# Performance work log

Hardware: AMD Instinct MI355X
Metric: run time of the kernel (lower is better)

Reference implementation:

```python
import jax, jax.numpy as jnp
import numpy as np

B, E, S, D = 32, 64, 50, 300   # batch, sentences/essay, words/sentence, word dim
F = 100                        # conv filters (cnn_lstm_convunits_size)
H = 100                        # lstm units (cnn_lstm_att_pool_size)
W_WIN = 5                      # word window length


def setup_inputs() -> dict:
    key = jax.random.key(0)
    ks = jax.random.split(key, 12)
    n = lambda k, shape: (jax.random.normal(k, shape, jnp.float32) * 0.05)
    return {
        "essays": jax.random.normal(ks[0], (B, E, S, D), jnp.float32),
        "conv_k": n(ks[1], (1, W_WIN, D, F)),      # HWIO
        "conv_b": jnp.zeros((F,), jnp.float32),
        "att1_mat": n(ks[2], (F, F)),
        "att1_bias": n(ks[3], (F,)),
        "att1_vec": n(ks[4], (F, 1)),
        "lstm_W": n(ks[5], (F + H, 4 * H)),        # TF BasicLSTMCell kernel, gate order i,j,f,o
        "lstm_b": jnp.zeros((4 * H,), jnp.float32),
        "att2_mat": n(ks[6], (H, H)),
        "att2_bias": n(ks[7], (H,)),
        "att2_vec": n(ks[8], (H, 1)),
        "dense_w": n(ks[9], (H, 1)),
        "dense_b": jnp.zeros((1,), jnp.float32),
    }


def reference(essays, conv_k, conv_b, att1_mat, att1_bias, att1_vec,
              lstm_W, lstm_b, att2_mat, att2_bias, att2_vec,
              dense_w, dense_b):
    # conv2d, kernel [1, w_window_len], SAME padding, relu  -> [B,E,S,F]
    conv1 = jax.lax.conv_general_dilated(
        essays, conv_k, window_strides=(1, 1), padding="SAME",
        dimension_numbers=("NHWC", "HWIO", "NHWC"))
    conv1 = jax.nn.relu(conv1 + conv_b)

    # attention pooling over words (axis=2)
    a1 = jnp.tanh(jnp.einsum("besf,fg->besg", conv1, att1_mat) + att1_bias)
    a1 = jnp.einsum("besg,go->beso", a1, att1_vec)          # [B,E,S,1]
    a1 = jax.nn.softmax(a1, axis=2)
    sent = jnp.sum(a1 * conv1, axis=2)                       # [B,E,F]

    # BasicLSTMCell (forget_bias=1.0, gate order i,j,f,o) over sentence axis
    hdim = lstm_b.shape[0] // 4
    bsz = essays.shape[0]

    def step(carry, xt):
        c, h = carry
        z = jnp.concatenate([xt, h], axis=1) @ lstm_W + lstm_b
        i, j, f, o = jnp.split(z, 4, axis=1)
        c = c * jax.nn.sigmoid(f + 1.0) + jax.nn.sigmoid(i) * jnp.tanh(j)
        h = jax.nn.sigmoid(o) * jnp.tanh(c)
        return (c, h), h

    init = (jnp.zeros((bsz, hdim), sent.dtype), jnp.zeros((bsz, hdim), sent.dtype))
    xs = jnp.swapaxes(sent, 0, 1)                            # [E,B,F]
    _, hs = jax.lax.scan(step, init, xs)
    lstm = jnp.swapaxes(hs, 0, 1)                            # [B,E,H]

    # attention pooling over sentences (axis=1)
    a2 = jnp.tanh(jnp.einsum("beh,hg->beg", lstm, att2_mat) + att2_bias)
    a2 = jnp.einsum("beg,go->beo", a2, att2_vec)             # [B,E,1]
    a2 = jax.nn.softmax(a2, axis=1)
    essay_repr = jnp.sum(a2 * lstm, axis=1)                  # [B,H]

    preds = jax.nn.sigmoid(essay_repr @ dense_w + dense_b).reshape(-1)  # [B]
    return preds
```

## Files before the change

### kernel.cpp

```cpp
#include <hip/hip_runtime.h>
#include <hip/hip_bf16.h>
#include <stdint.h>

#define Bsz 32
#define Esz 64
#define Ssz 50
#define Dsz 300
#define Fsz 100
#define Hsz 100
#define WWIN 5

#define PX   328
#define PC   136
#define KT_CONV 50
#define NTILES  7
#define NGRP 2214

typedef __attribute__((ext_vector_type(8))) short bf16x8;
typedef __attribute__((ext_vector_type(8))) unsigned short u16x8;
typedef __attribute__((ext_vector_type(4))) float f32x4;
typedef _Float16 half2_t __attribute__((ext_vector_type(2)));

union UH32 { unsigned int u; half2_t v; };
union UH16 { _Float16 h; unsigned short u; };

__device__ __forceinline__ float sigmoid_fast(float x) {
    return 1.0f / (1.0f + __expf(-x));
}
__device__ __forceinline__ float tanhf_fast(float x) {
    const float ax = fabsf(x);
    const float e = __expf(2.0f * ax);
    const float t = 1.0f - 2.0f / (e + 1.0f);
    return copysignf(t, x);
}

__device__ __forceinline__ unsigned short f2bf(float x) {
    union { __hip_bfloat16 h; unsigned short u; } cv;
    cv.h = __float2bfloat16(x);
    return cv.u;
}
__device__ __forceinline__ unsigned int f2bf2(float lo, float hi) {
    union { __hip_bfloat162 h2; unsigned int u; } cv;
    cv.h2 = __float22bfloat162_rn(make_float2(lo, hi));
    return cv.u;
}
__device__ __forceinline__ float bf2f(unsigned short b) {
    union { uint32_t u; float f; } v; v.u = ((uint32_t)b) << 16;
    return v.f;
}
__device__ __forceinline__ float dpp_bcast(float z, const int sel) {
    int r;
    switch (sel) {
        case 0: r = __builtin_amdgcn_mov_dpp(__builtin_bit_cast(int, z), 0x00, 0xf, 0xf, false); break;
        case 1: r = __builtin_amdgcn_mov_dpp(__builtin_bit_cast(int, z), 0x55, 0xf, 0xf, false); break;
        case 2: r = __builtin_amdgcn_mov_dpp(__builtin_bit_cast(int, z), 0xaa, 0xf, 0xf, false); break;
        default: r = __builtin_amdgcn_mov_dpp(__builtin_bit_cast(int, z), 0xff, 0xf, 0xf, false); break;
    }
    return __builtin_bit_cast(float, r);
}

#define N_BTGC (KT_CONV * 112 * 32)
#define N_BTGA (4 * 112 * 32)
#define N_BTGW (4 * 400 * 32)
#define N_BTGP (52 * 400)

__global__ __launch_bounds__(256) void prep_kernel(
    const float* __restrict__ conv_k, const float* __restrict__ att1_mat,
    const float* __restrict__ lstm_W,
    unsigned short* __restrict__ BtgC, unsigned short* __restrict__ BtgA,
    unsigned short* __restrict__ BtgW, unsigned int* __restrict__ BtgP)
{
    const int total = N_BTGC + N_BTGA + N_BTGW + N_BTGP;
    for (int i = blockIdx.x * 256 + threadIdx.x; i < total; i += gridDim.x * 256) {
        if (i < N_BTGC) {
            const int kt = i / (112 * 32);
            const int r  = i % (112 * 32);
            const int n  = r / 32;
            const int kk = r % 32;
            const int w  = kt / 10;
            const int d  = (kt % 10) * 32 + kk;
            float val = (d < Dsz && n < Fsz) ? conv_k[((size_t)w * Dsz + d) * Fsz + n] : 0.f;
            BtgC[i] = f2bf(val);
        } else if (i < N_BTGC + N_BTGA) {
            const int j  = i - N_BTGC;
            const int kt = j / (112 * 32);
            const int r  = j % (112 * 32);
            const int n  = r / 32;
            const int kk = r % 32;
            const int k  = kt * 32 + kk;
            float val = (k < Fsz && n < Fsz) ? att1_mat[(size_t)k * Fsz + n] : 0.f;
            BtgA[j] = f2bf(val);
        } else if (i < N_BTGC + N_BTGA + N_BTGW) {
            const int j  = i - N_BTGC - N_BTGA;
            const int kt = j / (400 * 32);
            const int r  = j % (400 * 32);
            const int n  = r / 32;
            const int kk = r % 32;
            const int k  = kt * 32 + kk;
            float val = (k < Fsz) ? lstm_W[(size_t)k * 400 + n] : 0.f;
            BtgW[j] = f2bf(val);
        } else {
            const int j   = i - N_BTGC - N_BTGA - N_BTGW;
            const int k2  = j / 400;
            const int col = j - k2 * 400;
            const int gate = col & 3;
            const int cell = col >> 2;
            const int src  = gate * 100 + cell;
            const int k0 = 2 * k2, k1 = 2 * k2 + 1;
            const float v0 = (k0 < Hsz) ? lstm_W[(size_t)(Fsz + k0) * 400 + src] : 0.f;
            const float v1 = (k1 < Hsz) ? lstm_W[(size_t)(Fsz + k1) * 400 + src] : 0.f;
            union { _Float16 h[2]; unsigned int u; } cv;
            cv.h[0] = (_Float16)v0;
            cv.h[1] = (_Float16)v1;
            BtgP[j] = cv.u;
        }
    }
}

template<int KT>
__device__ __forceinline__ void cv_loadB(
    const unsigned short* __restrict__ BtgC, const int (&boffs)[7], bf16x8 (&b)[7])
{
#pragma unroll
    for (int nt = 0; nt < 7; ++nt)
        b[nt] = *reinterpret_cast<const bf16x8*>(BtgC + KT * 3584 + boffs[nt]);
}

template<int KT>
__device__ __forceinline__ void cv_loadA(
    const unsigned short* b0p, const unsigned short* b1p, int abase, bf16x8 (&a)[2])
{
    constexpr int off = (KT / 10) * PX + (KT % 10) * 32;
    a[0] = *reinterpret_cast<const bf16x8*>(&b0p[abase + off]);
    a[1] = *reinterpret_cast<const bf16x8*>(&b1p[abase + off]);
}

__device__ __forceinline__ void cv_mfma(
    const bf16x8 (&a)[2], const bf16x8 (&b)[7], f32x4 (&acc)[2][7])
{
    __builtin_amdgcn_s_setprio(1);
#pragma unroll
    for (int nt = 0; nt < 7; ++nt) {
        acc[0][nt] = __builtin_amdgcn_mfma_f32_16x16x32_bf16(a[0], b[nt], acc[0][nt], 0, 0, 0);
        acc[1][nt] = __builtin_amdgcn_mfma_f32_16x16x32_bf16(a[1], b[nt], acc[1][nt], 0, 0, 0);
    }
    __builtin_amdgcn_s_setprio(0);
}

template<int KT>
struct CvLoop {
    static __device__ __forceinline__ void run(
        const unsigned short* __restrict__ BtgC, const int (&boffs)[7],
        const unsigned short* b0p, const unsigned short* b1p, int abase,
        bf16x8 (&B0)[7], bf16x8 (&B1)[7], bf16x8 (&B2)[7],
        bf16x8 (&aX)[2], bf16x8 (&aY)[2], f32x4 (&acc)[2][7])
    {
        if constexpr (KT + 1 < KT_CONV) {
            if constexpr ((KT & 1) == 0) cv_loadA<KT + 1>(b0p, b1p, abase, aY);
            else                         cv_loadA<KT + 1>(b0p, b1p, abase, aX);
        }
        if constexpr (KT + 2 < KT_CONV) {
            if constexpr ((KT + 2) % 3 == 0)      cv_loadB<KT + 2>(BtgC, boffs, B0);
            else if constexpr ((KT + 2) % 3 == 1) cv_loadB<KT + 2>(BtgC, boffs, B1);
            else                                  cv_loadB<KT + 2>(BtgC, boffs, B2);
        }
        if constexpr ((KT & 1) == 0) {
            if constexpr (KT % 3 == 0)      cv_mfma(aX, B0, acc);
            else if constexpr (KT % 3 == 1) cv_mfma(aX, B1, acc);
            else                            cv_mfma(aX, B2, acc);
        } else {
            if constexpr (KT % 3 == 0)      cv_mfma(aY, B0, acc);
            else if constexpr (KT % 3 == 1) cv_mfma(aY, B1, acc);
            else                            cv_mfma(aY, B2, acc);
        }
        CvLoop<KT + 1>::run(BtgC, boffs, b0p, b1p, abase, B0, B1, B2, aX, aY, acc);
    }
};
template<>
struct CvLoop<KT_CONV> {
    static __device__ __forceinline__ void run(
        const unsigned short* __restrict__, const int (&)[7],
        const unsigned short*, const unsigned short*, int,
        bf16x8 (&)[7], bf16x8 (&)[7], bf16x8 (&)[7],
        bf16x8 (&)[2], bf16x8 (&)[2], f32x4 (&)[2][7]) {}
};

__global__ __launch_bounds__(256, 2) void conv_att1_kernel(
    const float* __restrict__ essays,
    const unsigned short* __restrict__ BtgC,
    const unsigned short* __restrict__ BtgA,
    const float* __restrict__ conv_b,
    const float* __restrict__ att1_bias,
    const float* __restrict__ att1_vec,
    unsigned short* __restrict__ sent_bf)
{
    __shared__ __align__(16) unsigned short buf[2][54 * PX];
    __shared__ float u_s[2][64];
    __shared__ float alpha_s[2][64];

    const int be0 = blockIdx.x * 2;
    const int tid = threadIdx.x;
    const int lane = tid & 63;
    const int wid  = tid >> 6;
    const int ln   = lane & 15;
    const int qd   = lane >> 4;

    if (tid < 128) u_s[tid >> 6][tid & 63] = 0.f;

    const int m = wid * 16 + ln;
    const int abase = (m < Ssz ? m : Ssz - 1) * PX + 8 * qd;

    int boffs[7];
#pragma unroll
    for (int nt = 0; nt < 7; ++nt) boffs[nt] = (nt * 16 + ln) * 32 + 8 * qd;

    bf16x8 B0[7], B1[7], B2[7];
    cv_loadB<0>(BtgC, boffs, B0);
    cv_loadB<1>(BtgC, boffs, B1);

#pragma unroll
    for (int es = 0; es < 2; ++es) {
        const float* in_g = essays + (size_t)(be0 + es) * (Ssz * Dsz);
        float4 va[9], vb[9];
        int rr[9], cc[9];
        bool hv[9], fv[9], gv[9];
#pragma unroll
        for (int it = 0; it < 9; ++it) {
            const int g  = tid + it * 256;
            const int r  = g / 41;
            const int c8 = (g - r * 41) * 8;
            const int s  = r - 2;
            gv[it] = (g < NGRP);
            hv[it] = gv[it] && (s >= 0) && (s < Ssz) && (c8 < Dsz);
            fv[it] = hv[it] && (c8 + 8 <= Dsz);
            const float* base = in_g + (hv[it] ? (s * Dsz + c8) : 0);
            va[it] = *reinterpret_cast<const float4*>(base);
            vb[it] = *reinterpret_cast<const float4*>(fv[it] ? base + 4 : base);
            rr[it] = r; cc[it] = c8;
        }
#pragma unroll
        for (int it = 0; it < 9; ++it) {
            if (!gv[it]) continue;
            const float e0 = hv[it] ? va[it].x : 0.f;
            const float e1 = hv[it] ? va[it].y : 0.f;
            const float e2 = hv[it] ? va[it].z : 0.f;
            const float e3 = hv[it] ? va[it].w : 0.f;
            const float e4 = fv[it] ? vb[it].x : 0.f;
            const float e5 = fv[it] ? vb[it].y : 0.f;
            const float e6 = fv[it] ? vb[it].z : 0.f;
            const float e7 = fv[it] ? vb[it].w : 0.f;
            uint4 o;
            o.x = f2bf2(e0, e1);
            o.y = f2bf2(e2, e3);
            o.z = f2bf2(e4, e5);
            o.w = f2bf2(e6, e7);
            *reinterpret_cast<uint4*>(&buf[es][rr[it] * PX + cc[it]]) = o;
        }
    }
    __syncthreads();

    const unsigned short* b0p = buf[0];
    const unsigned short* b1p = buf[1];

    f32x4 acc[2][7];
#pragma unroll
    for (int es = 0; es < 2; ++es)
#pragma unroll
        for (int nt = 0; nt < 7; ++nt) acc[es][nt] = (f32x4)0.f;

    {
        bf16x8 aX[2], aY[2];
        cv_loadA<0>(b0p, b1p, abase, aX);
        CvLoop<0>::run(BtgC, boffs, b0p, b1p, abase, B0, B1, B2, aX, aY, acc);
    }
    __syncthreads();

#pragma unroll
    for (int nt = 0; nt < 7; ++nt) {
        const int n_g = nt * 16 + ln;
        const float bias = (n_g < Fsz) ? conv_b[n_g] : 0.f;
#pragma unroll
        for (int es = 0; es < 2; ++es) {
#pragma unroll
            for (int j = 0; j < 4; ++j) {
                const int m_row = wid * 16 + qd * 4 + j;
                buf[es][m_row * PC + n_g] = f2bf(fmaxf(acc[es][nt][j] + bias, 0.f));
            }
        }
    }
    for (int idx = tid; idx < 2 * 64 * 2; idx += 256) {
        const int es = idx >> 7;
        const int r2 = idx & 127;
        const int row = r2 >> 1;
        const int c = 112 + (r2 & 1) * 8;
        *reinterpret_cast<u16x8*>(&buf[es][row * PC + c]) = (u16x8)0;
    }
    __syncthreads();

    f32x4 acc2[2][7];
#pragma unroll
    for (int es = 0; es < 2; ++es)
#pragma unroll
        for (int nt = 0; nt < 7; ++nt) acc2[es][nt] = (f32x4)0.f;

    const int abase2 = (wid * 16 + ln) * PC + 8 * qd;
#pragma unroll
    for (int kt = 0; kt < 4; ++kt) {
        bf16x8 a[2];
        a[0] = *reinterpret_cast<const bf16x8*>(&b0p[abase2 + kt * 32]);
        a[1] = *reinterpret_cast<const bf16x8*>(&b1p[abase2 + kt * 32]);
        bf16x8 bb[7];
#pragma unroll
        for (int nt = 0; nt < 7; ++nt)
            bb[nt] = *reinterpret_cast<const bf16x8*>(BtgA + kt * 3584 + boffs[nt]);
        __builtin_amdgcn_s_setprio(1);
#pragma unroll
        for (int nt = 0; nt < 7; ++nt) {
            acc2[0][nt] = __builtin_amdgcn_mfma_f32_16x16x32_bf16(a[0], bb[nt], acc2[0][nt], 0, 0, 0);
            acc2[1][nt] = __builtin_amdgcn_mfma_f32_16x16x32_bf16(a[1], bb[nt], acc2[1][nt], 0, 0, 0);
        }
        __builtin_amdgcn_s_setprio(0);
    }

    {
        float bias_v[7], vec_v[7];
#pragma unroll
        for (int nt = 0; nt < 7; ++nt) {
            const int g = nt * 16 + ln;
            const bool ok = (g < Fsz);
            bias_v[nt] = ok ? att1_bias[g] : 0.f;
            vec_v[nt]  = ok ? att1_vec[g]  : 0.f;
        }
#pragma unroll
        for (int es = 0; es < 2; ++es) {
#pragma unroll
            for (int j = 0; j < 4; ++j) {
                const int m_row = wid * 16 + qd * 4 + j;
                float val = 0.f;
                if (m_row < Ssz) {
#pragma unroll
                    for (int nt = 0; nt < 7; ++nt) {
                        const int g = nt * 16 + ln;
                        if (g < Fsz)
                            val += tanhf_fast(acc2[es][nt][j] + bias_v[nt]) * vec_v[nt];
                    }
                }
                val += __shfl_xor(val, 1);
                val += __shfl_xor(val, 2);
                val += __shfl_xor(val, 4);
                val += __shfl_xor(val, 8);
                if (ln == 0 && m_row < Ssz) atomicAdd(&u_s[es][m_row], val);
            }
        }
    }
    __syncthreads();

    if (wid < 2) {
        const float uv = (lane < Ssz) ? u_s[wid][lane] : -1e30f;
        float m2 = uv;
#pragma unroll
        for (int off = 32; off > 0; off >>= 1) m2 = fmaxf(m2, __shfl_xor(m2, off));
        float e = (lane < Ssz) ? __expf(uv - m2) : 0.f;
        float sum = e;
#pragma unroll
        for (int off = 32; off > 0; off >>= 1) sum += __shfl_xor(sum, off);
        alpha_s[wid][lane] = e / sum;
    }
    __syncthreads();

    {
        const int es = tid >> 7;
        const int f  = tid & 127;
        unsigned short v = 0;
        if (f < Fsz) {
            float a = 0.f;
            for (int s = 0; s < Ssz; ++s) a += alpha_s[es][s] * bf2f(buf[es][s * PC + f]);
            v = f2bf(a);
        }
        sent_bf[(size_t)(be0 + es) * 128 + f] = v;
    }
}

__global__ __launch_bounds__(256) void xpart_kernel(
    const unsigned short* __restrict__ sent_bf,
    const unsigned short* __restrict__ BtgW,
    const float* __restrict__ lstm_b,
    float* __restrict__ xpartB)
{
    const int wid  = threadIdx.x >> 6;
    const int mt   = blockIdx.x * 4 + wid;
    const int lane = threadIdx.x & 63;
    const int ln   = lane & 15;
    const int qd   = lane >> 4;
    const int m0   = mt * 16;

    f32x4 acc[25];
#pragma unroll
    for (int nt = 0; nt < 25; ++nt) acc[nt] = (f32x4)0.f;

#pragma unroll
    for (int kt = 0; kt < 4; ++kt) {
        const bf16x8 a = *reinterpret_cast<const bf16x8*>(
            sent_bf + (size_t)(m0 + ln) * 128 + kt * 32 + 8 * qd);
#pragma unroll
        for (int nt = 0; nt < 25; ++nt) {
            const bf16x8 b = *reinterpret_cast<const bf16x8*>(
                BtgW + ((size_t)kt * 400 + nt * 16 + ln) * 32 + 8 * qd);
            acc[nt] = __builtin_amdgcn_mfma_f32_16x16x32_bf16(a, b, acc[nt], 0, 0, 0);
        }
    }

#pragma unroll
    for (int nt = 0; nt < 25; ++nt) {
        const int col = nt * 16 + ln;
        const int gate = col / 100;
        const int cell = col - gate * 100;
        const float bias = lstm_b[col];
        const int gi = cell * 4 + gate;
#pragma unroll
        for (int j = 0; j < 4; ++j) {
            const int row = m0 + qd * 4 + j;
            xpartB[(size_t)row * 400 + gi] = acc[nt][j] + bias;
        }
    }
}

__global__ __launch_bounds__(448) void lstm_att2_kernel(
    const float* __restrict__ xpartB,
    const unsigned int* __restrict__ BtgP,
    const float* __restrict__ att2_mat,
    const float* __restrict__ att2_bias,
    const float* __restrict__ att2_vec,
    const float* __restrict__ dense_w,
    const float* __restrict__ dense_b,
    float* __restrict__ out)
{
    __shared__ __align__(16) float xp_lds[Esz * 400];
    __shared__ __align__(16) float hist[Esz * Hsz];
    __shared__ __align__(16) unsigned short h16[2][104];
    __shared__ float u2_s[Esz];
    __shared__ float alpha2_s[Esz];
    __shared__ float repr_s[Hsz];

    const int b   = blockIdx.x;
    const int tid = threadIdx.x;
    const bool actv = tid < 400;
    const int cell = tid >> 2;
    const int g    = tid & 3;

    {
        const float4* src = reinterpret_cast<const float4*>(xpartB + (size_t)b * Esz * 400);
        float4* dst = reinterpret_cast<float4*>(xp_lds);
        for (int i = tid; i < Esz * 100; i += 448) dst[i] = src[i];
    }

    unsigned int wp[52];
    if (actv) {
#pragma unroll
        for (int q = 0; q < 52; ++q) wp[q] = BtgP[q * 400 + tid];
    }
    if (tid < 104) { h16[0][tid] = 0; h16[1][tid] = 0; }
    float c = 0.f;
    __syncthreads();

    for (int t = 0; t < Esz; ++t) {
        float z = 0.f;
        if (actv) {
            const uint4* hq = reinterpret_cast<const uint4*>(h16[t & 1]);
            float za = xp_lds[t * 400 + tid], zb = 0.f, zc = 0.f, zd = 0.f;
#pragma unroll
            for (int q = 0; q < 13; ++q) {
                const uint4 hv = hq[q];
                UH32 h0, h1, h2, h3, w0, w1, w2, w3;
                h0.u = hv.x; h1.u = hv.y; h2.u = hv.z; h3.u = hv.w;
                w0.u = wp[4 * q + 0]; w1.u = wp[4 * q + 1];
                w2.u = wp[4 * q + 2]; w3.u = wp[4 * q + 3];
                za = __builtin_amdgcn_fdot2(w0.v, h0.v, za, false);
                zb = __builtin_amdgcn_fdot2(w1.v, h1.v, zb, false);
                zc = __builtin_amdgcn_fdot2(w2.v, h2.v, zc, false);
                zd = __builtin_amdgcn_fdot2(w3.v, h3.v, zd, false);
            }
            z = (za + zb) + (zc + zd);

            const float zi = dpp_bcast(z, 0);
            const float zj = dpp_bcast(z, 1);
            const float zf = dpp_bcast(z, 2);
            const float zo = dpp_bcast(z, 3);

            c = c * sigmoid_fast(zf + 1.0f) + sigmoid_fast(zi) * tanhf_fast(zj);
            const float h = sigmoid_fast(zo) * tanhf_fast(c);
            if (g == 0) {
                UH16 cv; cv.h = (_Float16)h;
                h16[(t + 1) & 1][cell] = cv.u;
                hist[t * Hsz + cell] = h;
            }
        }
        __syncthreads();
    }

    float* w2_s = xp_lds;
    for (int idx = tid; idx < Esz * Hsz; idx += 448) {
        const int e = idx / Hsz;
        const int gg = idx - e * Hsz;
        const float* lp = hist + e * Hsz;
        float a0 = 0.f, a1 = 0.f, a2 = 0.f, a3 = 0.f;
        for (int k = 0; k < Hsz; k += 4) {
            a0 += lp[k + 0] * att2_mat[(k + 0) * Hsz + gg];
            a1 += lp[k + 1] * att2_mat[(k + 1) * Hsz + gg];
            a2 += lp[k + 2] * att2_mat[(k + 2) * Hsz + gg];
            a3 += lp[k + 3] * att2_mat[(k + 3) * Hsz + gg];
        }
        w2_s[idx] = tanhf_fast(att2_bias[gg] + ((a0 + a1) + (a2 + a3))) * att2_vec[gg];
    }
    __syncthreads();

    if (tid < Esz) {
        float acc = 0.f;
        const float* wpp = w2_s + tid * Hsz;
        for (int gg = 0; gg < Hsz; ++gg) acc += wpp[gg];
        u2_s[tid] = acc;
    }
    __syncthreads();

    if (tid < 64) {
        const float uv = u2_s[tid];
        float m = uv;
#pragma unroll
        for (int off = 32; off > 0; off >>= 1) m = fmaxf(m, __shfl_xor(m, off));
        float e = __expf(uv - m);
        float sum = e;
#pragma unroll
        for (int off = 32; off > 0; off >>= 1) sum += __shfl_xor(sum, off);
        alpha2_s[tid] = e / sum;
    }
    __syncthreads();

    if (tid < Hsz) {
        float acc = 0.f;
        for (int e = 0; e < Esz; ++e) acc += alpha2_s[e] * hist[e * Hsz + tid];
        repr_s[tid] = acc;
    }
    __syncthreads();

    if (tid == 0) {
        float acc = dense_b[0];
        for (int hh = 0; hh < Hsz; ++hh) acc += repr_s[hh] * dense_w[hh];
        out[b] = sigmoid_fast(acc);
    }
}

extern "C" void kernel_launch(void* const* d_in, const int* in_sizes, int n_in,
                              void* d_out, int out_size, void* d_ws, size_t ws_size,
                              hipStream_t stream) {
    const float* essays    = (const float*)d_in[0];
    const float* conv_k    = (const float*)d_in[1];
    const float* conv_b    = (const float*)d_in[2];
    const float* att1_mat  = (const float*)d_in[3];
    const float* att1_bias = (const float*)d_in[4];
    const float* att1_vec  = (const float*)d_in[5];
    const float* lstm_W    = (const float*)d_in[6];
    const float* lstm_b    = (const float*)d_in[7];
    const float* att2_mat  = (const float*)d_in[8];
    const float* att2_bias = (const float*)d_in[9];
    const float* att2_vec  = (const float*)d_in[10];
    const float* dense_w   = (const float*)d_in[11];
    const float* dense_b   = (const float*)d_in[12];

    float* out = (float*)d_out;

    char* ws = (char*)d_ws;
    unsigned short* sent_bf = (unsigned short*)ws;
    float* xpartB = (float*)(ws + 524288);
    unsigned short* BtgC = (unsigned short*)(ws + 3801088);
    unsigned short* BtgA = (unsigned short*)(ws + 4159488);
    unsigned short* BtgW = (unsigned short*)(ws + 4188160);
    unsigned int*   BtgP = (unsigned int*)(ws + 4290560);

    prep_kernel<<<512, 256, 0, stream>>>(conv_k, att1_mat, lstm_W, BtgC, BtgA, BtgW, BtgP);
    conv_att1_kernel<<<Bsz * Esz / 2, 256, 0, stream>>>(
        essays, BtgC, BtgA, conv_b, att1_bias, att1_vec, sent_bf);
    xpart_kernel<<<32, 256, 0, stream>>>(sent_bf, BtgW, lstm_b, xpartB);
    lstm_att2_kernel<<<Bsz, 448, 0, stream>>>(
        xpartB, BtgP, att2_mat, att2_bias, att2_vec, dense_w, dense_b, out);
}
```

Before: 223.9 us.

## Retile conv MFMA to 2x2 wave grid and halve LSTM threads per cell

The conv and att1 GEMMs move from each wave owning a 16-row M strip across 7 N tiles to a 2x2 wave grid. Each wave now owns 32 rows by 64 columns, with N padded to 128. This cuts redundant B-fragment loads per wave and raises A reuse, but adds padded columns and more accumulator registers. Separately, the LSTM recurrence kernel uses 2 threads per cell, each computing two gates, instead of 4. Gates are exchanged with a single DPP pair swap, and the block shrinks from 448 to 256 threads, which lowers the cost of the per-step barrier but doubles the dot-product work per thread.

```diff
diff --git a/kernel.cpp b/kernel.cpp
--- a/kernel.cpp
+++ b/kernel.cpp
@@ -13,7 +13,6 @@
 #define PX   328
 #define PC   136
 #define KT_CONV 50
-#define NTILES  7
 #define NGRP 2214
 
 typedef __attribute__((ext_vector_type(8))) short bf16x8;
@@ -48,19 +47,13 @@
     union { uint32_t u; float f; } v; v.u = ((uint32_t)b) << 16;
     return v.f;
 }
-__device__ __forceinline__ float dpp_bcast(float z, const int sel) {
-    int r;
-    switch (sel) {
-        case 0: r = __builtin_amdgcn_mov_dpp(__builtin_bit_cast(int, z), 0x00, 0xf, 0xf, false); break;
-        case 1: r = __builtin_amdgcn_mov_dpp(__builtin_bit_cast(int, z), 0x55, 0xf, 0xf, false); break;
-        case 2: r = __builtin_amdgcn_mov_dpp(__builtin_bit_cast(int, z), 0xaa, 0xf, 0xf, false); break;
-        default: r = __builtin_amdgcn_mov_dpp(__builtin_bit_cast(int, z), 0xff, 0xf, 0xf, false); break;
-    }
+__device__ __forceinline__ float dpp_swap_pair(float z) {
+    int r = __builtin_amdgcn_mov_dpp(__builtin_bit_cast(int, z), 0xB1, 0xf, 0xf, false);
     return __builtin_bit_cast(float, r);
 }
 
-#define N_BTGC (KT_CONV * 112 * 32)
-#define N_BTGA (4 * 112 * 32)
+#define N_BTGC (KT_CONV * 128 * 32)
+#define N_BTGA (4 * 128 * 32)
 #define N_BTGW (4 * 400 * 32)
 #define N_BTGP (52 * 400)
 
@@ -73,8 +66,8 @@
     const int total = N_BTGC + N_BTGA + N_BTGW + N_BTGP;
     for (int i = blockIdx.x * 256 + threadIdx.x; i < total; i += gridDim.x * 256) {
         if (i < N_BTGC) {
-            const int kt = i / (112 * 32);
-            const int r  = i % (112 * 32);
+            const int kt = i / (128 * 32);
+            const int r  = i % (128 * 32);
             const int n  = r / 32;
             const int kk = r % 32;
             const int w  = kt / 10;
@@ -83,8 +76,8 @@
             BtgC[i] = f2bf(val);
         } else if (i < N_BTGC + N_BTGA) {
             const int j  = i - N_BTGC;
-            const int kt = j / (112 * 32);
-            const int r  = j % (112 * 32);
+            const int kt = j / (128 * 32);
+            const int r  = j % (128 * 32);
             const int n  = r / 32;
             const int kk = r % 32;
             const int k  = kt * 32 + kk;
@@ -119,41 +112,48 @@
 
 template<int KT>
 __device__ __forceinline__ void cv_loadB(
-    const unsigned short* __restrict__ BtgC, const int (&boffs)[7], bf16x8 (&b)[7])
+    const unsigned short* __restrict__ BtgC, const int (&boffs)[4], bf16x8 (&b)[4])
 {
 #pragma unroll
-    for (int nt = 0; nt < 7; ++nt)
-        b[nt] = *reinterpret_cast<const bf16x8*>(BtgC + KT * 3584 + boffs[nt]);
+    for (int i = 0; i < 4; ++i)
+        b[i] = *reinterpret_cast<const bf16x8*>(BtgC + KT * 4096 + boffs[i]);
 }
 
 template<int KT>
 __device__ __forceinline__ void cv_loadA(
-    const unsigned short* b0p, const unsigned short* b1p, int abase, bf16x8 (&a)[2])
+    const unsigned short* b0p, const unsigned short* b1p,
+    const int (&abase)[2], bf16x8 (&a)[2][2])
 {
     constexpr int off = (KT / 10) * PX + (KT % 10) * 32;
-    a[0] = *reinterpret_cast<const bf16x8*>(&b0p[abase + off]);
-    a[1] = *reinterpret_cast<const bf16x8*>(&b1p[abase + off]);
+#pragma unroll
+    for (int mtl = 0; mtl < 2; ++mtl) {
+        a[0][mtl] = *reinterpret_cast<const bf16x8*>(&b0p[abase[mtl] + off]);
+        a[1][mtl] = *reinterpret_cast<const bf16x8*>(&b1p[abase[mtl] + off]);
+    }
 }
 
 __device__ __forceinline__ void cv_mfma(
-    const bf16x8 (&a)[2], const bf16x8 (&b)[7], f32x4 (&acc)[2][7])
+    const bf16x8 (&a)[2][2], const bf16x8 (&b)[4], f32x4 (&acc)[2][2][4])
 {
     __builtin_amdgcn_s_setprio(1);
 #pragma unroll
-    for (int nt = 0; nt < 7; ++nt) {
-        acc[0][nt] = __builtin_amdgcn_mfma_f32_16x16x32_bf16(a[0], b[nt], acc[0][nt], 0, 0, 0);
-        acc[1][nt] = __builtin_amdgcn_mfma_f32_16x16x32_bf16(a[1], b[nt], acc[1][nt], 0, 0, 0);
-    }
+    for (int es = 0; es < 2; ++es)
+#pragma unroll
+        for (int mtl = 0; mtl < 2; ++mtl)
+#pragma unroll
+            for (int i = 0; i < 4; ++i)
+                acc[es][mtl][i] = __builtin_amdgcn_mfma_f32_16x16x32_bf16(
+                    a[es][mtl], b[i], acc[es][mtl][i], 0, 0, 0);
     __builtin_amdgcn_s_setprio(0);
 }
 
 template<int KT>
 struct CvLoop {
     static __device__ __forceinline__ void run(
-        const unsigned short* __restrict__ BtgC, const int (&boffs)[7],
-        const unsigned short* b0p, const unsigned short* b1p, int abase,
-        bf16x8 (&B0)[7], bf16x8 (&B1)[7], bf16x8 (&B2)[7],
-        bf16x8 (&aX)[2], bf16x8 (&aY)[2], f32x4 (&acc)[2][7])
+        const unsigned short* __restrict__ BtgC, const int (&boffs)[4],
+        const unsigned short* b0p, const unsigned short* b1p, const int (&abase)[2],
+        bf16x8 (&B0)[4], bf16x8 (&B1)[4], bf16x8 (&B2)[4],
+        bf16x8 (&aX)[2][2], bf16x8 (&aY)[2][2], f32x4 (&acc)[2][2][4])
     {
         if constexpr (KT + 1 < KT_CONV) {
             if constexpr ((KT & 1) == 0) cv_loadA<KT + 1>(b0p, b1p, abase, aY);
@@ -179,10 +179,10 @@
 template<>
 struct CvLoop<KT_CONV> {
     static __device__ __forceinline__ void run(
-        const unsigned short* __restrict__, const int (&)[7],
-        const unsigned short*, const unsigned short*, int,
-        bf16x8 (&)[7], bf16x8 (&)[7], bf16x8 (&)[7],
-        bf16x8 (&)[2], bf16x8 (&)[2], f32x4 (&)[2][7]) {}
+        const unsigned short* __restrict__, const int (&)[4],
+        const unsigned short*, const unsigned short*, const int (&)[2],
+        bf16x8 (&)[4], bf16x8 (&)[4], bf16x8 (&)[4],
+        bf16x8 (&)[2][2], bf16x8 (&)[2][2], f32x4 (&)[2][2][4]) {}
 };
 
 __global__ __launch_bounds__(256, 2) void conv_att1_kernel(
@@ -204,17 +204,23 @@
     const int wid  = tid >> 6;
     const int ln   = lane & 15;
     const int qd   = lane >> 4;
+    const int mgrp = wid >> 1;
+    const int ngrp = wid & 1;
 
     if (tid < 128) u_s[tid >> 6][tid & 63] = 0.f;
 
-    const int m = wid * 16 + ln;
-    const int abase = (m < Ssz ? m : Ssz - 1) * PX + 8 * qd;
-
-    int boffs[7];
-#pragma unroll
-    for (int nt = 0; nt < 7; ++nt) boffs[nt] = (nt * 16 + ln) * 32 + 8 * qd;
-
-    bf16x8 B0[7], B1[7], B2[7];
+    int abase[2];
+#pragma unroll
+    for (int mtl = 0; mtl < 2; ++mtl) {
+        const int m = (mgrp * 2 + mtl) * 16 + ln;
+        abase[mtl] = (m < Ssz ? m : Ssz - 1) * PX + 8 * qd;
+    }
+    int boffs[4];
+#pragma unroll
+    for (int i = 0; i < 4; ++i)
+        boffs[i] = ((ngrp * 4 + i) * 16 + ln) * 32 + 8 * qd;
+
+    bf16x8 B0[4], B1[4], B2[4];
     cv_loadB<0>(BtgC, boffs, B0);
     cv_loadB<1>(BtgC, boffs, B1);
 
@@ -262,29 +268,36 @@
     const unsigned short* b0p = buf[0];
     const unsigned short* b1p = buf[1];
 
-    f32x4 acc[2][7];
+    f32x4 acc[2][2][4];
 #pragma unroll
     for (int es = 0; es < 2; ++es)
 #pragma unroll
-        for (int nt = 0; nt < 7; ++nt) acc[es][nt] = (f32x4)0.f;
+        for (int mtl = 0; mtl < 2; ++mtl)
+#pragma unroll
+            for (int i = 0; i < 4; ++i) acc[es][mtl][i] = (f32x4)0.f;
 
     {
-        bf16x8 aX[2], aY[2];
+        bf16x8 aX[2][2], aY[2][2];
         cv_loadA<0>(b0p, b1p, abase, aX);
         CvLoop<0>::run(BtgC, boffs, b0p, b1p, abase, B0, B1, B2, aX, aY, acc);
     }
     __syncthreads();
 
 #pragma unroll
-    for (int nt = 0; nt < 7; ++nt) {
-        const int n_g = nt * 16 + ln;
-        const float bias = (n_g < Fsz) ? conv_b[n_g] : 0.f;
-#pragma unroll
-        for (int es = 0; es < 2; ++es) {
-#pragma unroll
-            for (int j = 0; j < 4; ++j) {
-                const int m_row = wid * 16 + qd * 4 + j;
-                buf[es][m_row * PC + n_g] = f2bf(fmaxf(acc[es][nt][j] + bias, 0.f));
+    for (int i = 0; i < 4; ++i) {
+        const int n_g = (ngrp * 4 + i) * 16 + ln;
+        if (n_g < Fsz) {
+            const float bias = conv_b[n_g];
+#pragma unroll
+            for (int es = 0; es < 2; ++es) {
+#pragma unroll
+                for (int mtl = 0; mtl < 2; ++mtl) {
+#pragma unroll
+                    for (int j = 0; j < 4; ++j) {
+                        const int m_row = (mgrp * 2 + mtl) * 16 + qd * 4 + j;
+                        buf[es][m_row * PC + n_g] = f2bf(fmaxf(acc[es][mtl][i][j] + bias, 0.f));
+                    }
+                }
             }
         }
     }
@@ -297,59 +310,67 @@
     }
     __syncthreads();
 
-    f32x4 acc2[2][7];
+    f32x4 acc2[2][2][4];
 #pragma unroll
     for (int es = 0; es < 2; ++es)
 #pragma unroll
-        for (int nt = 0; nt < 7; ++nt) acc2[es][nt] = (f32x4)0.f;
-
-    const int abase2 = (wid * 16 + ln) * PC + 8 * qd;
-#pragma unroll
-    for (int kt = 0; kt < 4; ++kt) {
-        bf16x8 a[2];
-        a[0] = *reinterpret_cast<const bf16x8*>(&b0p[abase2 + kt * 32]);
-        a[1] = *reinterpret_cast<const bf16x8*>(&b1p[abase2 + kt * 32]);
-        bf16x8 bb[7];
-#pragma unroll
-        for (int nt = 0; nt < 7; ++nt)
-            bb[nt] = *reinterpret_cast<const bf16x8*>(BtgA + kt * 3584 + boffs[nt]);
-        __builtin_amdgcn_s_setprio(1);
-#pragma unroll
-        for (int nt = 0; nt < 7; ++nt) {
-            acc2[0][nt] = __builtin_amdgcn_mfma_f32_16x16x32_bf16(a[0], bb[nt], acc2[0][nt], 0, 0, 0);
-            acc2[1][nt] = __builtin_amdgcn_mfma_f32_16x16x32_bf16(a[1], bb[nt], acc2[1][nt], 0, 0, 0);
-        }
-        __builtin_amdgcn_s_setprio(0);
-    }
+        for (int mtl = 0; mtl < 2; ++mtl)
+#pragma unroll
+            for (int i = 0; i < 4; ++i) acc2[es][mtl][i] = (f32x4)0.f;
 
     {
-        float bias_v[7], vec_v[7];
-#pragma unroll
-        for (int nt = 0; nt < 7; ++nt) {
-            const int g = nt * 16 + ln;
+        int abase2[2];
+#pragma unroll
+        for (int mtl = 0; mtl < 2; ++mtl)
+            abase2[mtl] = ((mgrp * 2 + mtl) * 16 + ln) * PC + 8 * qd;
+
+#pragma unroll
+        for (int kt = 0; kt < 4; ++kt) {
+            bf16x8 a[2][2];
+#pragma unroll
+            for (int mtl = 0; mtl < 2; ++mtl) {
+                a[0][mtl] = *reinterpret_cast<const bf16x8*>(&b0p[abase2[mtl] + kt * 32]);
+                a[1][mtl] = *reinterpret_cast<const bf16x8*>(&b1p[abase2[mtl] + kt * 32]);
+            }
+            bf16x8 bb[4];
+#pragma unroll
+            for (int i = 0; i < 4; ++i)
+                bb[i] = *reinterpret_cast<const bf16x8*>(BtgA + kt * 4096 + boffs[i]);
+            cv_mfma(a, bb, acc2);
+        }
+    }
+
+    {
+        float bias_v[4], vec_v[4];
+#pragma unroll
+        for (int i = 0; i < 4; ++i) {
+            const int g = (ngrp * 4 + i) * 16 + ln;
             const bool ok = (g < Fsz);
-            bias_v[nt] = ok ? att1_bias[g] : 0.f;
-            vec_v[nt]  = ok ? att1_vec[g]  : 0.f;
+            bias_v[i] = ok ? att1_bias[g] : 0.f;
+            vec_v[i]  = ok ? att1_vec[g]  : 0.f;
         }
 #pragma unroll
         for (int es = 0; es < 2; ++es) {
 #pragma unroll
-            for (int j = 0; j < 4; ++j) {
-                const int m_row = wid * 16 + qd * 4 + j;
-                float val = 0.f;
-                if (m_row < Ssz) {
-#pragma unroll
-                    for (int nt = 0; nt < 7; ++nt) {
-                        const int g = nt * 16 + ln;
-                        if (g < Fsz)
-                            val += tanhf_fast(acc2[es][nt][j] + bias_v[nt]) * vec_v[nt];
+            for (int mtl = 0; mtl < 2; ++mtl) {
+#pragma unroll
+                for (int j = 0; j < 4; ++j) {
+                    const int m_row = (mgrp * 2 + mtl) * 16 + qd * 4 + j;
+                    float val = 0.f;
+                    if (m_row < Ssz) {
+#pragma unroll
+                        for (int i = 0; i < 4; ++i) {
+                            const int g = (ngrp * 4 + i) * 16 + ln;
+                            if (g < Fsz)
+                                val += tanhf_fast(acc2[es][mtl][i][j] + bias_v[i]) * vec_v[i];
+                        }
                     }
+                    val += __shfl_xor(val, 1);
+                    val += __shfl_xor(val, 2);
+                    val += __shfl_xor(val, 4);
+                    val += __shfl_xor(val, 8);
+                    if (ln == 0 && m_row < Ssz) atomicAdd(&u_s[es][m_row], val);
                 }
-                val += __shfl_xor(val, 1);
-                val += __shfl_xor(val, 2);
-                val += __shfl_xor(val, 4);
-                val += __shfl_xor(val, 8);
-                if (ln == 0 && m_row < Ssz) atomicAdd(&u_s[es][m_row], val);
             }
         }
     }
@@ -425,7 +446,7 @@
     }
 }
 
-__global__ __launch_bounds__(448) void lstm_att2_kernel(
+__global__ __launch_bounds__(256, 1) void lstm_att2_kernel(
     const float* __restrict__ xpartB,
     const unsigned int* __restrict__ BtgP,
     const float* __restrict__ att2_mat,
@@ -444,52 +465,64 @@
 
     const int b   = blockIdx.x;
     const int tid = threadIdx.x;
-    const bool actv = tid < 400;
-    const int cell = tid >> 2;
-    const int g    = tid & 3;
+    const bool actv = tid < 200;
+    const bool odd = tid & 1;
+    const int cell = tid >> 1;
 
     {
         const float4* src = reinterpret_cast<const float4*>(xpartB + (size_t)b * Esz * 400);
         float4* dst = reinterpret_cast<float4*>(xp_lds);
-        for (int i = tid; i < Esz * 100; i += 448) dst[i] = src[i];
-    }
-
-    unsigned int wp[52];
+        for (int i = tid; i < Esz * 100; i += 256) dst[i] = src[i];
+    }
+
+    uint2 wq[52];
     if (actv) {
 #pragma unroll
-        for (int q = 0; q < 52; ++q) wp[q] = BtgP[q * 400 + tid];
+        for (int q = 0; q < 52; ++q)
+            wq[q] = *reinterpret_cast<const uint2*>(BtgP + q * 400 + 2 * tid);
     }
     if (tid < 104) { h16[0][tid] = 0; h16[1][tid] = 0; }
     float c = 0.f;
     __syncthreads();
 
     for (int t = 0; t < Esz; ++t) {
-        float z = 0.f;
         if (actv) {
+            const float2 xp2 = *reinterpret_cast<const float2*>(&xp_lds[t * 400 + 2 * tid]);
             const uint4* hq = reinterpret_cast<const uint4*>(h16[t & 1]);
-            float za = xp_lds[t * 400 + tid], zb = 0.f, zc = 0.f, zd = 0.f;
+            float za0 = xp2.x, za1 = 0.f;
+            float zb0 = xp2.y, zb1 = 0.f;
 #pragma unroll
             for (int q = 0; q < 13; ++q) {
                 const uint4 hv = hq[q];
-                UH32 h0, h1, h2, h3, w0, w1, w2, w3;
+                UH32 h0, h1, h2, h3;
                 h0.u = hv.x; h1.u = hv.y; h2.u = hv.z; h3.u = hv.w;
-                w0.u = wp[4 * q + 0]; w1.u = wp[4 * q + 1];
-                w2.u = wp[4 * q + 2]; w3.u = wp[4 * q + 3];
-                za = __builtin_amdgcn_fdot2(w0.v, h0.v, za, false);
-                zb = __builtin_amdgcn_fdot2(w1.v, h1.v, zb, false);
-                zc = __builtin_amdgcn_fdot2(w2.v, h2.v, zc, false);
-                zd = __builtin_amdgcn_fdot2(w3.v, h3.v, zd, false);
+                UH32 wa0, wa1, wa2, wa3, wb0, wb1, wb2, wb3;
+                wa0.u = wq[4 * q + 0].x; wb0.u = wq[4 * q + 0].y;
+                wa1.u = wq[4 * q + 1].x; wb1.u = wq[4 * q + 1].y;
+                wa2.u = wq[4 * q + 2].x; wb2.u = wq[4 * q + 2].y;
+                wa3.u = wq[4 * q + 3].x; wb3.u = wq[4 * q + 3].y;
+                za0 = __builtin_amdgcn_fdot2(wa0.v, h0.v, za0, false);
+                za1 = __builtin_amdgcn_fdot2(wa1.v, h1.v, za1, false);
+                za0 = __builtin_amdgcn_fdot2(wa2.v, h2.v, za0, false);
+                za1 = __builtin_amdgcn_fdot2(wa3.v, h3.v, za1, false);
+                zb0 = __builtin_amdgcn_fdot2(wb0.v, h0.v, zb0, false);
+                zb1 = __builtin_amdgcn_fdot2(wb1.v, h1.v, zb1, false);
+                zb0 = __builtin_amdgcn_fdot2(wb2.v, h2.v, zb0, false);
+                zb1 = __builtin_amdgcn_fdot2(wb3.v, h3.v, zb1, false);
             }
-            z = (za + zb) + (zc + zd);
-
-            const float zi = dpp_bcast(z, 0);
-            const float zj = dpp_bcast(z, 1);
-            const float zf = dpp_bcast(z, 2);
-            const float zo = dpp_bcast(z, 3);
+            const float z0 = za0 + za1;
+            const float z1 = zb0 + zb1;
+
+            const float o0 = dpp_swap_pair(z0);
+            const float o1 = dpp_swap_pair(z1);
+            const float zi = odd ? o0 : z0;
+            const float zj = odd ? o1 : z1;
+            const float zf = odd ? z0 : o0;
+            const float zo = odd ? z1 : o1;
 
             c = c * sigmoid_fast(zf + 1.0f) + sigmoid_fast(zi) * tanhf_fast(zj);
             const float h = sigmoid_fast(zo) * tanhf_fast(c);
-            if (g == 0) {
+            if (!odd) {
                 UH16 cv; cv.h = (_Float16)h;
                 h16[(t + 1) & 1][cell] = cv.u;
                 hist[t * Hsz + cell] = h;
@@ -499,7 +532,7 @@
     }
 
     float* w2_s = xp_lds;
-    for (int idx = tid; idx < Esz * Hsz; idx += 448) {
+    for (int idx = tid; idx < Esz * Hsz; idx += 256) {
         const int e = idx / Hsz;
         const int gg = idx - e * Hsz;
         const float* lp = hist + e * Hsz;
@@ -572,14 +605,14 @@
     unsigned short* sent_bf = (unsigned short*)ws;
     float* xpartB = (float*)(ws + 524288);
     unsigned short* BtgC = (unsigned short*)(ws + 3801088);
-    unsigned short* BtgA = (unsigned short*)(ws + 4159488);
-    unsigned short* BtgW = (unsigned short*)(ws + 4188160);
-    unsigned int*   BtgP = (unsigned int*)(ws + 4290560);
+    unsigned short* BtgA = (unsigned short*)(ws + 4210688);
+    unsigned short* BtgW = (unsigned short*)(ws + 4243456);
+    unsigned int*   BtgP = (unsigned int*)(ws + 4345856);
 
     prep_kernel<<<512, 256, 0, stream>>>(conv_k, att1_mat, lstm_W, BtgC, BtgA, BtgW, BtgP);
     conv_att1_kernel<<<Bsz * Esz / 2, 256, 0, stream>>>(
         essays, BtgC, BtgA, conv_b, att1_bias, att1_vec, sent_bf);
     xpart_kernel<<<32, 256, 0, stream>>>(sent_bf, BtgW, lstm_b, xpartB);
-    lstm_att2_kernel<<<Bsz, 448, 0, stream>>>(
+    lstm_att2_kernel<<<Bsz, 256, 0, stream>>>(
         xpartB, BtgP, att2_mat, att2_bias, att2_vec, dense_w, dense_b, out);
 }
```

Result: faster. 204.9 us (-8.5%).
